# Performance work log

Hardware: AMD Instinct MI355X
Metric: run time of the kernel (lower is better)

## Reference

```python
import jax, jax.numpy as jnp
import numpy as np

D_MODEL = 1024
NUM_HEADS = 16
HEAD_DIM = D_MODEL // NUM_HEADS


def setup_inputs() -> dict:
    key = jax.random.key(0)
    ks = jax.random.split(key, 9)
    B, S, D = 4, 2048, D_MODEL
    scale = 1.0 / np.sqrt(D)
    x = jax.random.normal(ks[0], (B, S, D), dtype=jnp.float32)
    wq = jax.random.normal(ks[1], (D, D), dtype=jnp.float32) * scale
    wk = jax.random.normal(ks[2], (D, D), dtype=jnp.float32) * scale
    wv = jax.random.normal(ks[3], (D, D), dtype=jnp.float32) * scale
    wo = jax.random.normal(ks[4], (D, D), dtype=jnp.float32) * scale
    bq = jax.random.normal(ks[5], (D,), dtype=jnp.float32) * 0.02
    bk = jax.random.normal(ks[6], (D,), dtype=jnp.float32) * 0.02
    bv = jax.random.normal(ks[7], (D,), dtype=jnp.float32) * 0.02
    bo = jax.random.normal(ks[8], (D,), dtype=jnp.float32) * 0.02
    return {"x": x, "wq": wq, "bq": bq, "wk": wk, "bk": bk,
            "wv": wv, "bv": bv, "wo": wo, "bo": bo}


def _split_heads(t):  # [B,S,D] -> [B,H,S,Dh]
    B, S, _ = t.shape
    return t.reshape(B, S, NUM_HEADS, HEAD_DIM).transpose(0, 2, 1, 3)


def reference(x, wq, bq, wk, bk, wv, bv, wo, bo):
    B, S, D = x.shape
    q = _split_heads(x @ wq + bq)  # [B,H,S,Dh]
    k = _split_heads(x @ wk + bk)
    v = _split_heads(x @ wv + bv)
    scores = jnp.einsum("bhqd,bhkd->bhqk", q, k) / jnp.sqrt(
        jnp.asarray(HEAD_DIM, dtype=x.dtype))
    causal = jnp.tril(jnp.ones((S, S), dtype=bool))  # [S,S]
    scores = jnp.where(causal, scores, jnp.finfo(scores.dtype).min)
    attn = jax.nn.softmax(scores, axis=-1)
    ctx = jnp.einsum("bhqk,bhkd->bhqd", attn, v)  # [B,H,S,Dh]
    ctx = ctx.transpose(0, 2, 1, 3).reshape(B, S, D)
    return ctx @ wo + bo
```

## Files before the change

kernel.cpp:

```cpp
#include <hip/hip_runtime.h>
#include <hip/hip_bf16.h>
#include <stdint.h>

#define DMODEL 1024
#define NH 16
#define DH 64
#define BATCH 4
#define SEQ 2048

#if __has_builtin(__builtin_amdgcn_exp2f)
#define EXP2F(x) __builtin_amdgcn_exp2f(x)
#else
#define EXP2F(x) exp2f(x)
#endif

typedef __attribute__((ext_vector_type(8))) short short8;
typedef __attribute__((ext_vector_type(4))) float f32x4;
typedef __attribute__((ext_vector_type(4))) ushort ushort4v;

__device__ __forceinline__ ushort f2bf(float f) {
    union { float f; unsigned u; } v; v.f = f;
    unsigned r = v.u + 0x7fffu + ((v.u >> 16) & 1u);
    return (ushort)(r >> 16);
}

__global__ __launch_bounds__(256) void convert_bf16(const float* __restrict__ src,
                                                    ushort* __restrict__ dst) {
    const size_t i = ((size_t)blockIdx.x * 256 + threadIdx.x) * 8;
    float4 a = *(const float4*)(src + i);
    float4 b = *(const float4*)(src + i + 4);
    short8 r;
    r[0] = (short)f2bf(a.x); r[1] = (short)f2bf(a.y);
    r[2] = (short)f2bf(a.z); r[3] = (short)f2bf(a.w);
    r[4] = (short)f2bf(b.x); r[5] = (short)f2bf(b.y);
    r[6] = (short)f2bf(b.z); r[7] = (short)f2bf(b.w);
    *(short8*)(dst + i) = r;
}

__global__ __launch_bounds__(256) void transpose_cvt_w4(
    const float* __restrict__ s0, const float* __restrict__ s1,
    const float* __restrict__ s2, const float* __restrict__ s3,
    ushort* __restrict__ d0, ushort* __restrict__ d1,
    ushort* __restrict__ d2, ushort* __restrict__ d3) {
    __shared__ ushort tile[64][65];
    const int z = blockIdx.z;
    const float* src = (z == 0) ? s0 : (z == 1) ? s1 : (z == 2) ? s2 : s3;
    ushort* dst = (z == 0) ? d0 : (z == 1) ? d1 : (z == 2) ? d2 : d3;
    const int bx = blockIdx.x * 64;
    const int by = blockIdx.y * 64;
    const int tx = threadIdx.x & 63, ty = threadIdx.x >> 6;
    #pragma unroll
    for (int i = 0; i < 64; i += 4)
        tile[ty + i][tx] = f2bf(src[(size_t)(by + ty + i) * DMODEL + bx + tx]);
    __syncthreads();
    #pragma unroll
    for (int i = 0; i < 64; i += 4)
        dst[(size_t)(bx + ty + i) * DMODEL + by + tx] = tile[tx][ty + i];
}

#define BK 64
#define NT 16

template <int MODE>
__global__ __launch_bounds__(512, 2) void gemm_tile(
    const ushort* __restrict__ A, const ushort* __restrict__ Bt,
    const float* __restrict__ b0, const float* __restrict__ b1,
    const float* __restrict__ b2,
    void* __restrict__ o0v, void* __restrict__ o1v, void* __restrict__ o2v) {
    __shared__ __align__(16) ushort lds[73728];
    const int tid  = threadIdx.x;
    const int lane = tid & 63;
    const int wv   = tid >> 6;

    const int bid = blockIdx.x;
    const int by  = 4 * (bid & 7) + ((bid >> 3) & 3);
    const int bx  = bid >> 5;
    const int mBase = by * 256, nBase = bx * 128;

    const int wm = (wv >> 1) * 64;
    const int wn = (wv & 1) * 64;
    const int frow = lane & 15;
    const int fq   = lane >> 4;
    const int r7   = frow & 7;
    const int sw0  = (fq ^ r7) << 3;
    const int sw1  = ((4 + fq) ^ r7) << 3;

    const int trow = tid >> 3;
    const int tcho = ((tid & 7) ^ (trow & 7)) * 8;
    const ushort* gA = A  + (size_t)(mBase + trow) * DMODEL + tcho;
    const ushort* gB = Bt + (size_t)(nBase + trow) * DMODEL + tcho;
    const int ldsw = wv * 512;

    f32x4 acc[4][4];
    #pragma unroll
    for (int i = 0; i < 4; ++i)
        #pragma unroll
        for (int j = 0; j < 4; ++j) acc[i][j] = (f32x4){0.f, 0.f, 0.f, 0.f};

#define STG(gp, off) __builtin_amdgcn_global_load_lds( \
    (const __attribute__((address_space(1))) void*)(gp), \
    (__attribute__((address_space(3))) void*)&lds[(off) + ldsw], 16, 0, 0)
#define STAGE_A(sb, u, h) STG(gA + (size_t)(h) * 64 * DMODEL + (u) * BK, \
                              (sb) + (h) * 4096)
#define STAGE_B(sb, u, h) STG(gB + (size_t)(h) * 64 * DMODEL + (u) * BK, \
                              (sb) + 16384 + (h) * 4096)

    STAGE_A(0, 0, 0); STAGE_A(0, 0, 1); STAGE_A(0, 0, 2); STAGE_A(0, 0, 3);
    STAGE_B(0, 0, 0); STAGE_B(0, 0, 1);
    STAGE_A(24576, 1, 0); STAGE_A(24576, 1, 1); STAGE_A(24576, 1, 2);
    STAGE_A(24576, 1, 3); STAGE_B(24576, 1, 0); STAGE_B(24576, 1, 1);
    asm volatile("s_waitcnt vmcnt(6)" ::: "memory");
    __builtin_amdgcn_s_barrier();

    int sc = 0;
    #pragma unroll 1
    for (int u = 0; u < NT; ++u) {
        const int scB = sc * 24576;
        const int sp  = (sc == 0) ? 2 : sc - 1;
        const int spB = sp * 24576;
        const ushort* bufA = &lds[scB + wm * 64];
        const ushort* bufB = &lds[scB + 16384 + wn * 64];

        if (u + 2 < NT) {
            STAGE_A(spB, u + 2, 0); STAGE_A(spB, u + 2, 1);
            STAGE_A(spB, u + 2, 2); STAGE_A(spB, u + 2, 3);
            STAGE_B(spB, u + 2, 0); STAGE_B(spB, u + 2, 1);
        }

        short8 af[4][2], bf[4][2];
        #pragma unroll
        for (int f = 0; f < 4; ++f) {
            const int ro = (f * 16 + frow) * 64;
            af[f][0] = *(const short8*)&bufA[ro + sw0];
            af[f][1] = *(const short8*)&bufA[ro + sw1];
        }
        #pragma unroll
        for (int j = 0; j < 4; ++j) {
            const int ro = (j * 16 + frow) * 64;
            bf[j][0] = *(const short8*)&bufB[ro + sw0];
            bf[j][1] = *(const short8*)&bufB[ro + sw1];
        }
        __builtin_amdgcn_s_setprio(1);
        #pragma unroll
        for (int f = 0; f < 4; ++f)
            #pragma unroll
            for (int j = 0; j < 4; ++j)
                #pragma unroll
                for (int ks = 0; ks < 2; ++ks)
                    acc[f][j] = __builtin_amdgcn_mfma_f32_16x16x32_bf16(
                        af[f][ks], bf[j][ks], acc[f][j], 0, 0, 0);
        __builtin_amdgcn_s_setprio(0);

        if (u + 2 < NT)       { asm volatile("s_waitcnt vmcnt(6)" ::: "memory"); }
        else if (u + 2 == NT) { asm volatile("s_waitcnt vmcnt(0)" ::: "memory"); }
        __builtin_amdgcn_s_barrier();
        sc = (sc == 2) ? 0 : sc + 1;
    }
#undef STG
#undef STAGE_A
#undef STAGE_B

    const int orow = fq * 4;
    const int ocol = frow;

    if (MODE == 1) {
        #pragma unroll
        for (int i = 0; i < 4; ++i)
            #pragma unroll
            for (int j = 0; j < 4; ++j)
                #pragma unroll
                for (int r = 0; r < 4; ++r) {
                    const int m = mBase + wm + i * 16 + orow + r;
                    const int n = nBase + wn + j * 16 + ocol;
                    ((float*)o0v)[(size_t)m * DMODEL + n] = acc[i][j][r] + b0[n];
                }
        return;
    }

    __syncthreads();
    ushort* o0 = (ushort*)o0v; ushort* o1 = (ushort*)o1v; ushort* o2 = (ushort*)o2v;
    ushort* sw = &lds[wv * 1152];
    const int mat = nBase >> 10;
    const int nb0 = (nBase & 1023) + wn;
    const int hb  = nb0 >> 6;
    const float* bp = (mat == 0) ? b0 : ((mat == 1) ? b1 : b2);
    float bj[4];
    #pragma unroll
    for (int j = 0; j < 4; ++j) bj[j] = bp[nb0 + j * 16 + ocol];
    const int mrow = mBase + wm;
    const int bbq = mrow >> 11;
    const int s0w = mrow & 2047;
    const float qscale = (mat == 0) ? 0.1803368801f : 1.0f;

    if (mat < 2) {
        ushort* obase = ((mat == 0) ? o0 : o1) +
                        ((size_t)(bbq * NH + hb) * SEQ + s0w) * DH;
        const int row = lane >> 2, cc = lane & 3;
        #pragma unroll
        for (int i = 0; i < 4; ++i) {
            #pragma unroll
            for (int j = 0; j < 4; ++j)
                #pragma unroll
                for (int r = 0; r < 4; ++r)
                    sw[(orow + r) * 72 + j * 16 + ocol] =
                        f2bf((acc[i][j][r] + bj[j]) * qscale);
            asm volatile("s_waitcnt lgkmcnt(0)" ::: "memory");
            #pragma unroll
            for (int p = 0; p < 2; ++p) {
                short8 v8 = *(const short8*)&sw[row * 72 + cc * 8 + p * 32];
                *(short8*)&obase[(size_t)(i * 16 + row) * DH + cc * 8 + p * 32] = v8;
            }
            asm volatile("s_waitcnt lgkmcnt(0)" ::: "memory");
        }
    } else {
        const int rowd = lane >> 2, scl = lane & 3;
        #pragma unroll
        for (int j = 0; j < 4; ++j) {
            #pragma unroll
            for (int ii = 0; ii < 4; ++ii)
                #pragma unroll
                for (int r = 0; r < 4; ++r)
                    sw[ocol * 72 + ii * 16 + orow + r] = f2bf(acc[ii][j][r] + bj[j]);
            asm volatile("s_waitcnt lgkmcnt(0)" ::: "memory");
            ushort* vbase = o2 + ((size_t)(bbq * NH + hb) * DH + j * 16 + rowd) * SEQ + s0w;
            #pragma unroll
            for (int p = 0; p < 2; ++p) {
                short8 v8 = *(const short8*)&sw[rowd * 72 + scl * 8 + p * 32];
                *(short8*)&vbase[scl * 8 + p * 32] = v8;
            }
            asm volatile("s_waitcnt lgkmcnt(0)" ::: "memory");
        }
    }
}

#define PSTR 72
__global__ __launch_bounds__(512, 6) void flash_attn(
    const ushort* __restrict__ Q, const ushort* __restrict__ K,
    const ushort* __restrict__ Vt, ushort* __restrict__ ctx) {
    __shared__ __align__(16) ushort Ks[2][4096];
    __shared__ __align__(16) ushort Vs[2][4096];
    __shared__ __align__(16) ushort plds[8][16 * PSTR];
    const int tid  = threadIdx.x;
    const int lane = tid & 63;
    const int wv   = tid >> 6;
    const int bh   = blockIdx.x & 63;
    const int Jp   = blockIdx.x >> 6;
    const int bb = bh >> 4, h = bh & 15;

    const ushort* Qb = Q + (size_t)bh * SEQ * DH;
    const ushort* Kb = K + (size_t)bh * SEQ * DH;
    const ushort* Vb = Vt + (size_t)bh * DH * SEQ;

    const int frow = lane & 15;
    const int fq   = lane >> 4;
    const int trow = tid >> 3;
    const int tcho = ((tid & 7) ^ (trow & 7)) * 8;
    const int ldsw = wv * 512;

    short8 ones;
    #pragma unroll
    for (int i = 0; i < 8; ++i) ones[i] = (short)0x3F80;

#define FA_STG(gp, lp) __builtin_amdgcn_global_load_lds( \
    (const __attribute__((address_space(1))) void*)(gp), \
    (__attribute__((address_space(3))) void*)(lp), 16, 0, 0)

    #pragma unroll 1
    for (int half = 0; half < 2; ++half) {
        const int J = half ? (15 - Jp) : Jp;
        const int ktmax = 2 * J + 1;
        const int q0 = J * 128 + (wv >> 2) * 64 + (wv & 3) * 16;
        const int qmax = q0 + 15;

        short8 qf[2];
        #pragma unroll
        for (int ks = 0; ks < 2; ++ks)
            qf[ks] = *(const short8*)&Qb[(size_t)(q0 + frow) * DH + ks * 32 + fq * 8];

        f32x4 o[4], lacc;
        #pragma unroll
        for (int t = 0; t < 4; ++t) o[t] = (f32x4){0.f, 0.f, 0.f, 0.f};
        lacc = (f32x4){0.f, 0.f, 0.f, 0.f};

        FA_STG(Kb + (size_t)trow * DH + tcho, &Ks[0][ldsw]);
        FA_STG(Vb + (size_t)trow * SEQ + tcho, &Vs[0][ldsw]);
        asm volatile("s_waitcnt vmcnt(0)" ::: "memory");
        __builtin_amdgcn_s_barrier();

        #pragma unroll 1
        for (int kt = 0; kt <= ktmax; ++kt) {
            const int k0 = kt * 64;
            const int cur = kt & 1;
            if (kt < ktmax) {
                const int kn = k0 + 64;
                FA_STG(Kb + (size_t)(kn + trow) * DH + tcho, &Ks[cur ^ 1][ldsw]);
                FA_STG(Vb + (size_t)trow * SEQ + kn + tcho, &Vs[cur ^ 1][ldsw]);
            }
            const ushort* Ksc = Ks[cur];
            const ushort* Vsc = Vs[cur];

            if (k0 <= qmax) {
            if (k0 + 64 <= q0) {
                f32x4 sacc[4];
                #pragma unroll
                for (int nt = 0; nt < 4; ++nt) sacc[nt] = (f32x4){0.f, 0.f, 0.f, 0.f};
                #pragma unroll
                for (int nt = 0; nt < 4; ++nt) {
                    const int row = nt * 16 + frow, r7 = row & 7;
                    #pragma unroll
                    for (int ks = 0; ks < 2; ++ks) {
                        short8 kf = *(const short8*)
                            &Ksc[(row >> 3) * 512 + r7 * 64 + (((ks * 4 + fq) ^ r7) * 8)];
                        sacc[nt] = __builtin_amdgcn_mfma_f32_16x16x32_bf16(kf, qf[ks],
                                                                          sacc[nt], 0, 0, 0);
                    }
                }
                #pragma unroll
                for (int nt = 0; nt < 4; ++nt) {
                    float p0 = EXP2F(sacc[nt][0]);
                    float p1 = EXP2F(sacc[nt][1]);
                    float p2 = EXP2F(sacc[nt][2]);
                    float p3 = EXP2F(sacc[nt][3]);
                    uint2 dw;
                    dw.x = __builtin_amdgcn_perm(__float_as_uint(p1), __float_as_uint(p0),
                                                 0x07060302u);
                    dw.y = __builtin_amdgcn_perm(__float_as_uint(p3), __float_as_uint(p2),
                                                 0x07060302u);
                    *(uint2*)&plds[wv][frow * PSTR + nt * 16 + fq * 4] = dw;
                }
                asm volatile("s_waitcnt lgkmcnt(0)" ::: "memory");
                #pragma unroll
                for (int kc = 0; kc < 2; ++kc) {
                    short8 pf = *(const short8*)&plds[wv][frow * PSTR + kc * 32 + fq * 8];
                    lacc = __builtin_amdgcn_mfma_f32_16x16x32_bf16(ones, pf, lacc, 0, 0, 0);
                    __builtin_amdgcn_s_setprio(1);
                    #pragma unroll
                    for (int t = 0; t < 4; ++t) {
                        const int row = t * 16 + frow, r7 = row & 7;
                        short8 vf = *(const short8*)
                            &Vsc[(row >> 3) * 512 + r7 * 64 + (((kc * 4 + fq) ^ r7) * 8)];
                        o[t] = __builtin_amdgcn_mfma_f32_16x16x32_bf16(vf, pf, o[t], 0, 0, 0);
                    }
                    __builtin_amdgcn_s_setprio(0);
                }
            } else {
                const int qrow = q0 + frow;
                f32x4 sacc[4];
                #pragma unroll
                for (int nt = 0; nt < 4; ++nt) sacc[nt] = (f32x4){0.f, 0.f, 0.f, 0.f};
                #pragma unroll
                for (int nt = 0; nt < 4; ++nt)
                    if (k0 + nt * 16 <= qmax) {
                        const int row = nt * 16 + frow, r7 = row & 7;
                        #pragma unroll
                        for (int ks = 0; ks < 2; ++ks) {
                            short8 kf = *(const short8*)
                                &Ksc[(row >> 3) * 512 + r7 * 64 + (((ks * 4 + fq) ^ r7) * 8)];
                            sacc[nt] = __builtin_amdgcn_mfma_f32_16x16x32_bf16(kf, qf[ks],
                                                                              sacc[nt], 0, 0, 0);
                        }
                    }
                #pragma unroll
                for (int nt = 0; nt < 4; ++nt) {
                    uint2 dw; dw.x = 0u; dw.y = 0u;
                    if (k0 + nt * 16 <= qmax) {
                        float pp[4];
                        #pragma unroll
                        for (int r = 0; r < 4; ++r) {
                            const float e = EXP2F(sacc[nt][r]);
                            pp[r] = (k0 + nt * 16 + fq * 4 + r <= qrow) ? e : 0.f;
                        }
                        dw.x = __builtin_amdgcn_perm(__float_as_uint(pp[1]),
                                                     __float_as_uint(pp[0]), 0x07060302u);
                        dw.y = __builtin_amdgcn_perm(__float_as_uint(pp[3]),
                                                     __float_as_uint(pp[2]), 0x07060302u);
                    }
                    *(uint2*)&plds[wv][frow * PSTR + nt * 16 + fq * 4] = dw;
                }
                asm volatile("s_waitcnt lgkmcnt(0)" ::: "memory");
                #pragma unroll
                for (int kc = 0; kc < 2; ++kc) {
                    if (k0 + kc * 32 <= qmax) {
                        short8 pf = *(const short8*)&plds[wv][frow * PSTR + kc * 32 + fq * 8];
                        lacc = __builtin_amdgcn_mfma_f32_16x16x32_bf16(ones, pf, lacc, 0, 0, 0);
                        #pragma unroll
                        for (int t = 0; t < 4; ++t) {
                            const int row = t * 16 + frow, r7 = row & 7;
                            short8 vf = *(const short8*)
                                &Vsc[(row >> 3) * 512 + r7 * 64 + (((kc * 4 + fq) ^ r7) * 8)];
                            o[t] = __builtin_amdgcn_mfma_f32_16x16x32_bf16(vf, pf, o[t], 0, 0, 0);
                        }
                    }
                }
            }
            }

            asm volatile("s_waitcnt lgkmcnt(0) vmcnt(0)" ::: "memory");
            __builtin_amdgcn_s_barrier();
        }

        const float inv = 1.0f / lacc[0];
        const int qrow = q0 + frow;
        ushort* cp = ctx + (size_t)(bb * SEQ + qrow) * DMODEL + h * DH;
        #pragma unroll
        for (int t = 0; t < 4; ++t) {
            ushort4v ov;
            #pragma unroll
            for (int r = 0; r < 4; ++r) ov[r] = f2bf(o[t][r] * inv);
            *(ushort4v*)&cp[t * 16 + fq * 4] = ov;
        }
    }
#undef FA_STG
}

extern "C" void kernel_launch(void* const* d_in, const int* in_sizes, int n_in,
                              void* d_out, int out_size, void* d_ws, size_t ws_size,
                              hipStream_t stream) {
    const float* x  = (const float*)d_in[0];
    const float* wq = (const float*)d_in[1];
    const float* bq = (const float*)d_in[2];
    const float* wk = (const float*)d_in[3];
    const float* bk = (const float*)d_in[4];
    const float* wvp = (const float*)d_in[5];
    const float* bv = (const float*)d_in[6];
    const float* wo = (const float*)d_in[7];
    const float* bo = (const float*)d_in[8];
    float* out = (float*)d_out;
    ushort* ws = (ushort*)d_ws;

    const size_t QSZ = (size_t)BATCH * NH * SEQ * DH;
    ushort* xbf   = ws;
    ushort* qws   = ws + QSZ;
    ushort* kws   = ws + 2 * QSZ;
    ushort* vtws  = ws + 3 * QSZ;
    ushort* ctxws = ws + 4 * QSZ;
    ushort* wtqkv = ws + 5 * QSZ;
    ushort* wto   = wtqkv + 3 * (size_t)DMODEL * DMODEL;

    dim3 tb(256);
    convert_bf16<<<dim3(4096), tb, 0, stream>>>(x, xbf);
    transpose_cvt_w4<<<dim3(16, 16, 4), tb, 0, stream>>>(
        wq, wk, wvp, wo,
        wtqkv, wtqkv + (size_t)DMODEL * DMODEL, wtqkv + 2 * (size_t)DMODEL * DMODEL, wto);

    gemm_tile<0><<<dim3(768), dim3(512), 0, stream>>>(xbf, wtqkv, bq, bk, bv,
                                                      qws, kws, vtws);
    flash_attn<<<dim3(512), dim3(512), 0, stream>>>(qws, kws, vtws, ctxws);
    gemm_tile<1><<<dim3(256), dim3(512), 0, stream>>>(ctxws, wto, bo, nullptr, nullptr,
                                                      out, nullptr, nullptr);
}
```

Before: 242.5 us.

## Shrink GEMM tiles to 128x128 with BK=32 and 256-thread blocks

The projection GEMMs now use a 128x128 output tile with a K step of 32 instead of 256x128 with a K step of 64. Blocks drop to 4 waves and a smaller three-stage LDS ring, and the grid doubles. The swizzled LDS layout and the global-to-LDS mapping are redone so each row pair packs into 64-element rows. The aim is more blocks and higher occupancy per CU for better latency hiding, at the cost of less operand reuse per tile and twice as many barrier iterations.

```diff
diff --git a/kernel.cpp b/kernel.cpp
--- a/kernel.cpp
+++ b/kernel.cpp
@@ -58,37 +58,38 @@
         dst[(size_t)(bx + ty + i) * DMODEL + by + tx] = tile[tx][ty + i];
 }
 
-#define BK 64
-#define NT 16
+#define BK 32
+#define NT 32
 
 template <int MODE>
-__global__ __launch_bounds__(512, 2) void gemm_tile(
+__global__ __launch_bounds__(256, 3) void gemm_tile(
     const ushort* __restrict__ A, const ushort* __restrict__ Bt,
     const float* __restrict__ b0, const float* __restrict__ b1,
     const float* __restrict__ b2,
     void* __restrict__ o0v, void* __restrict__ o1v, void* __restrict__ o2v) {
-    __shared__ __align__(16) ushort lds[73728];
+    __shared__ __align__(16) ushort lds[24576];
     const int tid  = threadIdx.x;
     const int lane = tid & 63;
     const int wv   = tid >> 6;
 
     const int bid = blockIdx.x;
-    const int by  = 4 * (bid & 7) + ((bid >> 3) & 3);
-    const int bx  = bid >> 5;
-    const int mBase = by * 256, nBase = bx * 128;
+    const int by  = ((bid & 7) << 3) | ((bid >> 3) & 7);
+    const int bx  = bid >> 6;
+    const int mBase = by * 128, nBase = bx * 128;
 
     const int wm = (wv >> 1) * 64;
     const int wn = (wv & 1) * 64;
     const int frow = lane & 15;
     const int fq   = lane >> 4;
-    const int r7   = frow & 7;
-    const int sw0  = (fq ^ r7) << 3;
-    const int sw1  = ((4 + fq) ^ r7) << 3;
-
-    const int trow = tid >> 3;
-    const int tcho = ((tid & 7) ^ (trow & 7)) * 8;
-    const ushort* gA = A  + (size_t)(mBase + trow) * DMODEL + tcho;
-    const ushort* gB = Bt + (size_t)(nBase + trow) * DMODEL + tcho;
+    const int cA   = ((((fq << 1) | (frow & 1)) ^ (frow >> 1)) & 7) << 3;
+    const int roff = (frow >> 1) * 64 + cA;
+
+    const int sr   = tid >> 3;
+    const int bsw  = (tid & 7) ^ (sr & 7);
+    const int grow = (sr << 1) | (bsw & 1);
+    const int gkc8 = (bsw >> 1) * 8;
+    const ushort* gA = A  + (size_t)(mBase + grow) * DMODEL + gkc8;
+    const ushort* gB = Bt + (size_t)(nBase + grow) * DMODEL + gkc8;
     const int ldsw = wv * 512;
 
     f32x4 acc[4][4];
@@ -101,57 +102,47 @@
     (const __attribute__((address_space(1))) void*)(gp), \
     (__attribute__((address_space(3))) void*)&lds[(off) + ldsw], 16, 0, 0)
 #define STAGE_A(sb, u, h) STG(gA + (size_t)(h) * 64 * DMODEL + (u) * BK, \
-                              (sb) + (h) * 4096)
+                              (sb) + (h) * 2048)
 #define STAGE_B(sb, u, h) STG(gB + (size_t)(h) * 64 * DMODEL + (u) * BK, \
-                              (sb) + 16384 + (h) * 4096)
-
-    STAGE_A(0, 0, 0); STAGE_A(0, 0, 1); STAGE_A(0, 0, 2); STAGE_A(0, 0, 3);
-    STAGE_B(0, 0, 0); STAGE_B(0, 0, 1);
-    STAGE_A(24576, 1, 0); STAGE_A(24576, 1, 1); STAGE_A(24576, 1, 2);
-    STAGE_A(24576, 1, 3); STAGE_B(24576, 1, 0); STAGE_B(24576, 1, 1);
-    asm volatile("s_waitcnt vmcnt(6)" ::: "memory");
+                              (sb) + 4096 + (h) * 2048)
+
+    STAGE_A(0, 0, 0); STAGE_A(0, 0, 1); STAGE_B(0, 0, 0); STAGE_B(0, 0, 1);
+    STAGE_A(8192, 1, 0); STAGE_A(8192, 1, 1);
+    STAGE_B(8192, 1, 0); STAGE_B(8192, 1, 1);
+    asm volatile("s_waitcnt vmcnt(4)" ::: "memory");
     __builtin_amdgcn_s_barrier();
 
     int sc = 0;
     #pragma unroll 1
     for (int u = 0; u < NT; ++u) {
-        const int scB = sc * 24576;
+        const int scB = sc * 8192;
         const int sp  = (sc == 0) ? 2 : sc - 1;
-        const int spB = sp * 24576;
-        const ushort* bufA = &lds[scB + wm * 64];
-        const ushort* bufB = &lds[scB + 16384 + wn * 64];
+        const int spB = sp * 8192;
+        const ushort* bufA = &lds[scB + wm * 32];
+        const ushort* bufB = &lds[scB + 4096 + wn * 32];
 
         if (u + 2 < NT) {
             STAGE_A(spB, u + 2, 0); STAGE_A(spB, u + 2, 1);
-            STAGE_A(spB, u + 2, 2); STAGE_A(spB, u + 2, 3);
             STAGE_B(spB, u + 2, 0); STAGE_B(spB, u + 2, 1);
         }
 
-        short8 af[4][2], bf[4][2];
-        #pragma unroll
-        for (int f = 0; f < 4; ++f) {
-            const int ro = (f * 16 + frow) * 64;
-            af[f][0] = *(const short8*)&bufA[ro + sw0];
-            af[f][1] = *(const short8*)&bufA[ro + sw1];
-        }
-        #pragma unroll
-        for (int j = 0; j < 4; ++j) {
-            const int ro = (j * 16 + frow) * 64;
-            bf[j][0] = *(const short8*)&bufB[ro + sw0];
-            bf[j][1] = *(const short8*)&bufB[ro + sw1];
-        }
+        short8 af[4], bf[4];
+        #pragma unroll
+        for (int f = 0; f < 4; ++f)
+            af[f] = *(const short8*)&bufA[f * 512 + roff];
+        #pragma unroll
+        for (int j = 0; j < 4; ++j)
+            bf[j] = *(const short8*)&bufB[j * 512 + roff];
         __builtin_amdgcn_s_setprio(1);
         #pragma unroll
         for (int f = 0; f < 4; ++f)
             #pragma unroll
             for (int j = 0; j < 4; ++j)
-                #pragma unroll
-                for (int ks = 0; ks < 2; ++ks)
-                    acc[f][j] = __builtin_amdgcn_mfma_f32_16x16x32_bf16(
-                        af[f][ks], bf[j][ks], acc[f][j], 0, 0, 0);
+                acc[f][j] = __builtin_amdgcn_mfma_f32_16x16x32_bf16(
+                    af[f], bf[j], acc[f][j], 0, 0, 0);
         __builtin_amdgcn_s_setprio(0);
 
-        if (u + 2 < NT)       { asm volatile("s_waitcnt vmcnt(6)" ::: "memory"); }
+        if (u + 2 < NT)       { asm volatile("s_waitcnt vmcnt(4)" ::: "memory"); }
         else if (u + 2 == NT) { asm volatile("s_waitcnt vmcnt(0)" ::: "memory"); }
         __builtin_amdgcn_s_barrier();
         sc = (sc == 2) ? 0 : sc + 1;
@@ -443,9 +434,9 @@
         wq, wk, wvp, wo,
         wtqkv, wtqkv + (size_t)DMODEL * DMODEL, wtqkv + 2 * (size_t)DMODEL * DMODEL, wto);
 
-    gemm_tile<0><<<dim3(768), dim3(512), 0, stream>>>(xbf, wtqkv, bq, bk, bv,
-                                                      qws, kws, vtws);
+    gemm_tile<0><<<dim3(1536), tb, 0, stream>>>(xbf, wtqkv, bq, bk, bv,
+                                                qws, kws, vtws);
     flash_attn<<<dim3(512), dim3(512), 0, stream>>>(qws, kws, vtws, ctxws);
-    gemm_tile<1><<<dim3(256), dim3(512), 0, stream>>>(ctxws, wto, bo, nullptr, nullptr,
-                                                      out, nullptr, nullptr);
-}
+    gemm_tile<1><<<dim3(512), tb, 0, stream>>>(ctxws, wto, bo, nullptr, nullptr,
+                                               out, nullptr, nullptr);
+}
```

Result: no change. 245.2 us (+1.1%).
